# Kernel optimization log

Measured on AMD Instinct MI355X. Metric: run time of the kernel, lower is better.

## Reference

```python
import jax, jax.numpy as jnp
import numpy as np

B, S, D, H = 2, 2048, 2048, 16  # batch, seq, d_model, n_heads
LN_EPS = 1e-6  # flax nn.LayerNorm default


def _layernorm(x, scale):
    mu = jnp.mean(x, axis=-1, keepdims=True)
    var = jnp.var(x, axis=-1, keepdims=True)
    return (x - mu) * jax.lax.rsqrt(var + LN_EPS) * scale


def setup_inputs() -> dict:
    key = jax.random.key(0)
    ks = jax.random.split(key, 5)
    x = jax.random.normal(ks[0], (B, S, D), dtype=jnp.float32)
    # ALiBi-style bias, broadcastable over batch and query positions
    attn_bias = jax.random.normal(ks[1], (1, H, 1, S), dtype=jnp.float32)
    attention_mask = jnp.ones((B, S), dtype=jnp.int32)
    w_qkv = jax.random.normal(ks[2], (D, 3 * D), dtype=jnp.float32) * 0.01
    b_qkv = jnp.zeros((3 * D,), dtype=jnp.float32)
    wo = jax.random.normal(ks[3], (D, D), dtype=jnp.float32) * 0.01
    b_wo = jnp.zeros((D,), dtype=jnp.float32)
    q_ln_scale = jnp.ones((D,), dtype=jnp.float32)
    k_ln_scale = jnp.ones((D,), dtype=jnp.float32)
    return {"x": x, "attn_bias": attn_bias, "attention_mask": attention_mask,
            "w_qkv": w_qkv, "b_qkv": b_qkv, "wo": wo, "b_wo": b_wo,
            "q_ln_scale": q_ln_scale, "k_ln_scale": k_ln_scale}


def reference(x, attn_bias, attention_mask, w_qkv, b_qkv, wo, b_wo, q_ln_scale, k_ln_scale):
    b, s, ds = x.shape
    h = H
    d = ds // h  # head dim
    qkv = jnp.einsum('bsd,df->bsf', x, w_qkv) + b_qkv
    q, k, v = jnp.split(qkv, 3, axis=-1)
    # qk-LayerNorm is over the FULL d_model, before head split (as in source)
    q = _layernorm(q, q_ln_scale)
    k = _layernorm(k, k_ln_scale)
    q = q.reshape(b, s, h, d)
    k = k.reshape(b, s, h, d)
    v = v.reshape(b, s, h, d)
    atw = jnp.einsum('bqhd,bkhd->bhqk', q, k) * jax.lax.rsqrt(jnp.asarray(d, v.dtype))
    atw = atw + attn_bias  # ALiBi bias
    mv = jnp.finfo(atw.dtype).min
    # causal mask [1,1,s,s]
    causal = jnp.tril(jnp.ones((s, s), dtype=bool))[None, None]
    # padding mask: 0 where attended, min where masked
    pad = jnp.where(attention_mask.reshape(b, 1, 1, s) == 1, 0.0, mv).astype(atw.dtype)
    atw = atw + pad
    atw = atw + jnp.where(causal, 0.0, mv).astype(atw.dtype)
    atw = jax.nn.softmax(atw, axis=-1)
    out = jnp.einsum('bhqk,bkhd->bqhd', atw, v).reshape(b, s, ds)
    return jnp.einsum('bsd,de->bse', out, wo) + b_wo
```

## Files before the change

### kernel.cpp

```cpp
#include <hip/hip_runtime.h>
#include <stdint.h>
#include <stddef.h>


typedef __attribute__((ext_vector_type(8))) short bf16x8;
typedef __attribute__((ext_vector_type(4))) float f32x4;

#define MFMA16(a, b, c) __builtin_amdgcn_mfma_f32_16x16x32_bf16((a), (b), (c), 0, 0, 0)

__device__ __forceinline__ void async_copy16(void* lds, const void* g) {
  __builtin_amdgcn_global_load_lds(
      (const __attribute__((address_space(1))) void*)g,
      (__attribute__((address_space(3))) void*)lds, 16, 0, 0);
}

__device__ __forceinline__ short f2bf(float f) {
  union { float f; uint32_t u; } v; v.f = f;
  uint32_t r = (v.u + 0x7fffu + ((v.u >> 16) & 1u)) >> 16;
  return (short)(uint16_t)r;
}

__device__ __forceinline__ float bf2f(short s) {
  union { float f; uint32_t u; } v;
  v.u = ((uint32_t)(uint16_t)s) << 16;
  return v.f;
}

#define ATT_SCALE 0.08838834764831845f
#define VMDRAIN asm volatile("s_waitcnt vmcnt(0)" ::: "memory")

__global__ __launch_bounds__(256) void cvt_f32_bf16(const float* __restrict__ in,
                                                    short* __restrict__ out) {
  size_t i = ((size_t)blockIdx.x * 256 + threadIdx.x) * 8;
  f32x4 a = *(const f32x4*)(in + i);
  f32x4 b = *(const f32x4*)(in + i + 4);
  bf16x8 o;
#pragma unroll
  for (int j = 0; j < 4; ++j) { o[j] = f2bf(a[j]); o[4 + j] = f2bf(b[j]); }
  *(bf16x8*)(out + i) = o;
}

__global__ __launch_bounds__(256) void transpose_cvt(const float* __restrict__ in,
                                                     short* __restrict__ out,
                                                     int R, int C) {
  __shared__ float t[64][65];
  const int tid = threadIdx.x;
  const int c0 = blockIdx.x * 64, r0 = blockIdx.y * 64;
#pragma unroll
  for (int i = 0; i < 16; ++i) {
    int idx = i * 256 + tid;
    int r = idx >> 6, c = idx & 63;
    t[r][c] = in[(size_t)(r0 + r) * C + c0 + c];
  }
  __syncthreads();
#pragma unroll
  for (int i = 0; i < 16; ++i) {
    int idx = i * 256 + tid;
    int cc = idx >> 6, rr = idx & 63;
    out[(size_t)(c0 + cc) * R + r0 + rr] = f2bf(t[rr][cc]);
  }
}

__global__ __launch_bounds__(256) void transpose_v_bf(const short* __restrict__ qkv,
                                                      short* __restrict__ vt) {
  __shared__ short t[64][65];
  const int tid = threadIdx.x;
  const int d0 = blockIdx.x * 64;
  const int s0 = blockIdx.y * 64;
  const int bh = blockIdx.z;
  const int b = bh >> 4, h = bh & 15;
#pragma unroll
  for (int i = 0; i < 16; ++i) {
    int idx = i * 256 + tid;
    int r = idx >> 6, c = idx & 63;
    t[r][c] = qkv[(size_t)(b * 2048 + s0 + r) * 6144 + 4096 + h * 128 + d0 + c];
  }
  __syncthreads();
#pragma unroll
  for (int i = 0; i < 16; ++i) {
    int idx = i * 256 + tid;
    int dd = idx >> 6, ss = idx & 63;
    vt[((size_t)(bh * 128 + d0 + dd)) * 2048 + s0 + ss] = t[ss][dd];
  }
}

__global__ __launch_bounds__(256) void ln_qk(const short* __restrict__ qkv,
                                             const float* __restrict__ qsc,
                                             const float* __restrict__ ksc,
                                             short* __restrict__ q_bf,
                                             short* __restrict__ k_bf) {
  __shared__ float redS[2][4], redQ[2][4];
  const int row = blockIdx.x, tid = threadIdx.x;
  const int lane = tid & 63, wave = tid >> 6;
  const short* base = qkv + (size_t)row * 6144;
#pragma unroll
  for (int part = 0; part < 2; ++part) {
    const short* p = base + part * 2048 + tid * 8;
    bf16x8 v8 = *(const bf16x8*)p;
    float f[8];
#pragma unroll
    for (int j = 0; j < 8; ++j) f[j] = bf2f(v8[j]);
    float s = 0.f, sq = 0.f;
#pragma unroll
    for (int j = 0; j < 8; ++j) { s += f[j]; sq += f[j] * f[j]; }
#pragma unroll
    for (int d = 1; d < 64; d <<= 1) { s += __shfl_xor(s, d); sq += __shfl_xor(sq, d); }
    if (lane == 0) { redS[part][wave] = s; redQ[part][wave] = sq; }
    __syncthreads();
    float tot  = redS[part][0] + redS[part][1] + redS[part][2] + redS[part][3];
    float totq = redQ[part][0] + redQ[part][1] + redQ[part][2] + redQ[part][3];
    float mean = tot * (1.f / 2048.f);
    float var  = totq * (1.f / 2048.f) - mean * mean;
    float rstd = rsqrtf(var + 1e-6f) * (part == 0 ? ATT_SCALE : 1.0f);
    const float* scp = (part == 0 ? qsc : ksc) + tid * 8;
    f32x4 s0 = *(const f32x4*)scp;
    f32x4 s1 = *(const f32x4*)(scp + 4);
    bf16x8 o;
#pragma unroll
    for (int j = 0; j < 4; ++j) {
      o[j]     = f2bf((f[j] - mean) * rstd * s0[j]);
      o[4 + j] = f2bf((f[4 + j] - mean) * rstd * s1[j]);
    }
    short* outp = (part == 0 ? q_bf : k_bf) + (size_t)row * 2048 + tid * 8;
    *(bf16x8*)outp = o;
  }
}

template <typename OutT>
__global__ __launch_bounds__(256, 2) void gemm_bt_bias(const short* __restrict__ A,
                                                       const short* __restrict__ BT,
                                                       const float* __restrict__ bias,
                                                       OutT* __restrict__ C,
                                                       int M, int N, int K) {
  __shared__ alignas(16) short a_lds[128 * 64];
  __shared__ alignas(16) short b_lds[128 * 64];
  const int tid = threadIdx.x;
  const int lane = tid & 63, wave = tid >> 6;
  const int wr = wave >> 1, wc = wave & 1;
  const int tn = blockIdx.x, tm = blockIdx.y;
  const int r15 = lane & 15, hi = lane >> 4;

  const short* Ab = A + (size_t)tm * 128 * K;
  const short* Bb = BT + (size_t)tn * 128 * K;

  f32x4 acc[4][4];
  const f32x4 Z = {0.f, 0.f, 0.f, 0.f};
#pragma unroll
  for (int m = 0; m < 4; ++m)
#pragma unroll
    for (int n = 0; n < 4; ++n) acc[m][n] = Z;

  for (int k0 = 0; k0 < K; k0 += 64) {
    __syncthreads();
#pragma unroll
    for (int j = 0; j < 4; ++j) {
      int c = j * 256 + tid;
      int row = c >> 3;
      int ch = (c & 7) ^ (row & 7);
      async_copy16(&a_lds[c << 3], Ab + (size_t)row * K + k0 + (ch << 3));
      async_copy16(&b_lds[c << 3], Bb + (size_t)row * K + k0 + (ch << 3));
    }
    VMDRAIN;
    __syncthreads();
#pragma unroll
    for (int kk = 0; kk < 2; ++kk) {
      bf16x8 af[4], bfr[4];
#pragma unroll
      for (int m = 0; m < 4; ++m) {
        int row = wr * 64 + m * 16 + r15;
        af[m] = *(const bf16x8*)&a_lds[row * 64 + (((kk * 4 + hi) ^ (row & 7)) << 3)];
      }
#pragma unroll
      for (int n = 0; n < 4; ++n) {
        int row = wc * 64 + n * 16 + r15;
        bfr[n] = *(const bf16x8*)&b_lds[row * 64 + (((kk * 4 + hi) ^ (row & 7)) << 3)];
      }
#pragma unroll
      for (int m = 0; m < 4; ++m)
#pragma unroll
        for (int n = 0; n < 4; ++n)
          acc[m][n] = MFMA16(af[m], bfr[n], acc[m][n]);
    }
  }

  const int r0 = tm * 128 + wr * 64;
  const int c0 = tn * 128 + wc * 64;
#pragma unroll
  for (int n = 0; n < 4; ++n) {
    float bv = bias[c0 + n * 16 + r15];
#pragma unroll
    for (int m = 0; m < 4; ++m) {
#pragma unroll
      for (int r = 0; r < 4; ++r) {
        float val = acc[m][n][r] + bv;
        size_t idx = (size_t)(r0 + m * 16 + hi * 4 + r) * N + c0 + n * 16 + r15;
        if constexpr (sizeof(OutT) == 2) C[idx] = (OutT)f2bf(val);
        else                             C[idx] = val;
      }
    }
  }
}

__global__ __launch_bounds__(256) void attn_fwd(const short* __restrict__ q_bf,
                                                const short* __restrict__ k_bf,
                                                const short* __restrict__ vt,
                                                const float* __restrict__ abias,
                                                const int* __restrict__ amask,
                                                short* __restrict__ out_bf) {
  __shared__ alignas(16) short K_lds[64 * 128];
  __shared__ alignas(16) short V_lds[128 * 64];
  __shared__ alignas(16) short p_lds[4][16 * 64];
  __shared__ float bias_c[2048];

  const int tid = threadIdx.x, lane = tid & 63, wave = tid >> 6;
  const int qt = 31 - blockIdx.x;
  const int h = blockIdx.y, b = blockIdx.z;
  const int r15 = lane & 15, hi = lane >> 4;

  for (int i = tid; i < 2048; i += 256) {
    float bb = abias[h * 2048 + i];
    if (amask[b * 2048 + i] == 0) bb = -1e30f;
    bias_c[i] = bb;
  }

  const int qrow = b * 2048 + qt * 64 + wave * 16 + r15;
  bf16x8 qf[4];
#pragma unroll
  for (int kb = 0; kb < 4; ++kb)
    qf[kb] = *(const bf16x8*)(q_bf + (size_t)qrow * 2048 + h * 128 + kb * 32 + hi * 8);

  f32x4 O[8];
  const f32x4 Z = {0.f, 0.f, 0.f, 0.f};
#pragma unroll
  for (int n = 0; n < 8; ++n) O[n] = Z;
  f32x4 Ol = Z;
  float m_run[4];
#pragma unroll
  for (int r = 0; r < 4; ++r) m_run[r] = -3e38f;

  const short one_bf = (short)0x3F80;
  const bf16x8 ones_f = {one_bf, one_bf, one_bf, one_bf,
                         one_bf, one_bf, one_bf, one_bf};
  const int qg0 = qt * 64 + wave * 16 + hi * 4;
  const int ntiles = qt + 1;

  for (int kt = 0; kt < ntiles; ++kt) {
    __syncthreads();

#pragma unroll
    for (int j = 0; j < 4; ++j) {
      int c = j * 256 + tid;
      int kr = c >> 4, kc = (c & 15) ^ (kr & 7);
      async_copy16(&K_lds[c << 3],
                   k_bf + (size_t)(b * 2048 + kt * 64 + kr) * 2048 + h * 128 + (kc << 3));
      int vr = c >> 3, vc = (c & 7) ^ (vr & 7);
      async_copy16(&V_lds[c << 3],
                   vt + ((size_t)((b * 16 + h) * 128 + vr)) * 2048 + kt * 64 + (vc << 3));
    }
    VMDRAIN;
    __syncthreads();

    f32x4 s[4];
#pragma unroll
    for (int ks = 0; ks < 4; ++ks) {
      s[ks] = Z;
#pragma unroll
      for (int kb = 0; kb < 4; ++kb) {
        int row = ks * 16 + r15;
        int ch = (kb * 4 + hi) ^ (row & 7);
        bf16x8 kf = *(const bf16x8*)&K_lds[row * 128 + ch * 8];
        s[ks] = MFMA16(qf[kb], kf, s[ks]);
      }
    }

    if (kt == qt) {
#pragma unroll
      for (int ks = 0; ks < 4; ++ks) {
        int kg = kt * 64 + ks * 16 + r15;
        float bb = bias_c[kg];
#pragma unroll
        for (int r = 0; r < 4; ++r) {
          float v = s[ks][r] + bb;
          if (kg > qg0 + r) v = -1e30f;
          s[ks][r] = v;
        }
      }
    } else {
#pragma unroll
      for (int ks = 0; ks < 4; ++ks) {
        float bb = bias_c[kt * 64 + ks * 16 + r15];
#pragma unroll
        for (int r = 0; r < 4; ++r) s[ks][r] += bb;
      }
    }

    float corr[4];
#pragma unroll
    for (int r = 0; r < 4; ++r) {
      float mx = fmaxf(fmaxf(s[0][r], s[1][r]), fmaxf(s[2][r], s[3][r]));
      mx = fmaxf(mx, __shfl_xor(mx, 1));
      mx = fmaxf(mx, __shfl_xor(mx, 2));
      mx = fmaxf(mx, __shfl_xor(mx, 4));
      mx = fmaxf(mx, __shfl_xor(mx, 8));
      float mn = fmaxf(m_run[r], mx);
      corr[r] = __expf(m_run[r] - mn);
      m_run[r] = mn;
#pragma unroll
      for (int ks = 0; ks < 4; ++ks) s[ks][r] = __expf(s[ks][r] - mn);
    }
#pragma unroll
    for (int r = 0; r < 4; ++r) {
      Ol[r] *= corr[r];
#pragma unroll
      for (int n = 0; n < 8; ++n) O[n][r] *= corr[r];
    }

    short* pw = &p_lds[wave][0];
#pragma unroll
    for (int r = 0; r < 4; ++r) {
      int q = hi * 4 + r;
      int qs = (q & 7) << 3;
      uint32_t pk0, pk1;
      asm("v_cvt_pk_bf16_f32 %0, %1, %2" : "=v"(pk0) : "v"(s[0][r]), "v"(s[1][r]));
      asm("v_cvt_pk_bf16_f32 %0, %1, %2" : "=v"(pk1) : "v"(s[2][r]), "v"(s[3][r]));
      pw[q * 64 + ((r15) ^ qs)]      = (short)pk0;
      pw[q * 64 + ((16 + r15) ^ qs)] = (short)(pk0 >> 16);
      pw[q * 64 + ((32 + r15) ^ qs)] = (short)pk1;
      pw[q * 64 + ((48 + r15) ^ qs)] = (short)(pk1 >> 16);
    }

    bf16x8 pf[2];
#pragma unroll
    for (int kb = 0; kb < 2; ++kb)
      pf[kb] = *(const bf16x8*)&pw[r15 * 64 + ((kb * 32 + hi * 8) ^ ((r15 & 7) << 3))];

#pragma unroll
    for (int n = 0; n < 8; ++n) {
#pragma unroll
      for (int kb = 0; kb < 2; ++kb) {
        int row = n * 16 + r15;
        int ch = (kb * 4 + hi) ^ (row & 7);
        bf16x8 vf = *(const bf16x8*)&V_lds[row * 64 + ch * 8];
        O[n] = MFMA16(pf[kb], vf, O[n]);
      }
    }
    Ol = MFMA16(pf[0], ones_f, Ol);
    Ol = MFMA16(pf[1], ones_f, Ol);
  }

  float inv[4];
#pragma unroll
  for (int r = 0; r < 4; ++r) inv[r] = 1.0f / Ol[r];
  const int orow = b * 2048 + qt * 64 + wave * 16;
#pragma unroll
  for (int n = 0; n < 8; ++n)
#pragma unroll
    for (int r = 0; r < 4; ++r)
      out_bf[(size_t)(orow + hi * 4 + r) * 2048 + h * 128 + n * 16 + r15] =
          f2bf(O[n][r] * inv[r]);
}

extern "C" void kernel_launch(void* const* d_in, const int* in_sizes, int n_in,
                              void* d_out, int out_size, void* d_ws, size_t ws_size,
                              hipStream_t stream) {
  const float* x     = (const float*)d_in[0];
  const float* abias = (const float*)d_in[1];
  const int*   amask = (const int*)d_in[2];
  const float* w_qkv = (const float*)d_in[3];
  const float* b_qkv = (const float*)d_in[4];
  const float* wo    = (const float*)d_in[5];
  const float* b_wo  = (const float*)d_in[6];
  const float* q_ln  = (const float*)d_in[7];
  const float* k_ln  = (const float*)d_in[8];
  float* out = (float*)d_out;

  char* ws = (char*)d_ws;
  short* x_bf   = (short*)(ws);
  short* wqkvT  = (short*)(ws + 16777216);
  short* woT    = (short*)(ws + 41943040);
  short* q_bf   = (short*)(ws + 50331648);
  short* k_bf   = (short*)(ws + 67108864);
  short* vt     = (short*)(ws + 83886080);
  short* out_bf = (short*)(ws + 100663296);
  short* qkv_bf = (short*)(ws + 117440512);

  cvt_f32_bf16<<<4096, 256, 0, stream>>>(x, x_bf);
  transpose_cvt<<<dim3(96, 32), 256, 0, stream>>>(w_qkv, wqkvT, 2048, 6144);
  transpose_cvt<<<dim3(32, 32), 256, 0, stream>>>(wo, woT, 2048, 2048);
  gemm_bt_bias<short><<<dim3(48, 32), 256, 0, stream>>>(x_bf, wqkvT, b_qkv, qkv_bf,
                                                        4096, 6144, 2048);
  ln_qk<<<4096, 256, 0, stream>>>(qkv_bf, q_ln, k_ln, q_bf, k_bf);
  transpose_v_bf<<<dim3(2, 32, 32), 256, 0, stream>>>(qkv_bf, vt);
  attn_fwd<<<dim3(32, 16, 2), 256, 0, stream>>>(q_bf, k_bf, vt, abias, amask, out_bf);
  gemm_bt_bias<float><<<dim3(16, 32), 256, 0, stream>>>(out_bf, woT, b_wo, out,
                                                        4096, 2048, 2048);
}
```

Baseline: 357.3 us.

## Load K/V fragments directly from global memory instead of staging through LDS

The attention kernel no longer stages K and V tiles into shared memory with async copies and barriers. Each wave now reads its MFMA operands straight from global memory (relying on L2/cache), and reads the bias and mask per tile instead of precomputing a bias array in LDS. This removes the per-tile barriers and LDS traffic, and the lower LDS use may allow more blocks per CU. The cost is that each of the four waves redundantly fetches the same K/V data from global memory, and per-lane loads are strided by row.

```diff
diff --git a/kernel.cpp b/kernel.cpp
--- a/kernel.cpp
+++ b/kernel.cpp
@@ -201,27 +201,18 @@
   }
 }
 
-__global__ __launch_bounds__(256) void attn_fwd(const short* __restrict__ q_bf,
-                                                const short* __restrict__ k_bf,
-                                                const short* __restrict__ vt,
-                                                const float* __restrict__ abias,
-                                                const int* __restrict__ amask,
-                                                short* __restrict__ out_bf) {
-  __shared__ alignas(16) short K_lds[64 * 128];
-  __shared__ alignas(16) short V_lds[128 * 64];
+__global__ __launch_bounds__(256) void attn_fwd2(const short* __restrict__ q_bf,
+                                                 const short* __restrict__ k_bf,
+                                                 const short* __restrict__ vt,
+                                                 const float* __restrict__ abias,
+                                                 const int* __restrict__ amask,
+                                                 short* __restrict__ out_bf) {
   __shared__ alignas(16) short p_lds[4][16 * 64];
-  __shared__ float bias_c[2048];
 
   const int tid = threadIdx.x, lane = tid & 63, wave = tid >> 6;
   const int qt = 31 - blockIdx.x;
   const int h = blockIdx.y, b = blockIdx.z;
   const int r15 = lane & 15, hi = lane >> 4;
-
-  for (int i = tid; i < 2048; i += 256) {
-    float bb = abias[h * 2048 + i];
-    if (amask[b * 2048 + i] == 0) bb = -1e30f;
-    bias_c[i] = bb;
-  }
 
   const int qrow = b * 2048 + qt * 64 + wave * 16 + r15;
   bf16x8 qf[4];
@@ -244,31 +235,21 @@
   const int qg0 = qt * 64 + wave * 16 + hi * 4;
   const int ntiles = qt + 1;
 
+  const short* Kbase = k_bf + ((size_t)(b * 2048)) * 2048 + h * 128;
+  const short* Vbase = vt + ((size_t)((b * 16 + h) * 128)) * 2048;
+  const float* Bbase = abias + (size_t)h * 2048;
+  const int*   Mbase = amask + (size_t)b * 2048;
+
   for (int kt = 0; kt < ntiles; ++kt) {
-    __syncthreads();
-
-#pragma unroll
-    for (int j = 0; j < 4; ++j) {
-      int c = j * 256 + tid;
-      int kr = c >> 4, kc = (c & 15) ^ (kr & 7);
-      async_copy16(&K_lds[c << 3],
-                   k_bf + (size_t)(b * 2048 + kt * 64 + kr) * 2048 + h * 128 + (kc << 3));
-      int vr = c >> 3, vc = (c & 7) ^ (vr & 7);
-      async_copy16(&V_lds[c << 3],
-                   vt + ((size_t)((b * 16 + h) * 128 + vr)) * 2048 + kt * 64 + (vc << 3));
-    }
-    VMDRAIN;
-    __syncthreads();
-
     f32x4 s[4];
 #pragma unroll
     for (int ks = 0; ks < 4; ++ks) {
       s[ks] = Z;
+      const int krow = kt * 64 + ks * 16 + r15;
+      const short* kp = Kbase + (size_t)krow * 2048;
 #pragma unroll
       for (int kb = 0; kb < 4; ++kb) {
-        int row = ks * 16 + r15;
-        int ch = (kb * 4 + hi) ^ (row & 7);
-        bf16x8 kf = *(const bf16x8*)&K_lds[row * 128 + ch * 8];
+        bf16x8 kf = *(const bf16x8*)(kp + (kb * 4 + hi) * 8);
         s[ks] = MFMA16(qf[kb], kf, s[ks]);
       }
     }
@@ -277,7 +258,8 @@
 #pragma unroll
       for (int ks = 0; ks < 4; ++ks) {
         int kg = kt * 64 + ks * 16 + r15;
-        float bb = bias_c[kg];
+        float bb = Bbase[kg];
+        if (Mbase[kg] == 0) bb = -1e30f;
 #pragma unroll
         for (int r = 0; r < 4; ++r) {
           float v = s[ks][r] + bb;
@@ -288,7 +270,9 @@
     } else {
 #pragma unroll
       for (int ks = 0; ks < 4; ++ks) {
-        float bb = bias_c[kt * 64 + ks * 16 + r15];
+        int kg = kt * 64 + ks * 16 + r15;
+        float bb = Bbase[kg];
+        if (Mbase[kg] == 0) bb = -1e30f;
 #pragma unroll
         for (int r = 0; r < 4; ++r) s[ks][r] += bb;
       }
@@ -336,11 +320,11 @@
 
 #pragma unroll
     for (int n = 0; n < 8; ++n) {
+      const int vrow = n * 16 + r15;
+      const short* vp = Vbase + (size_t)vrow * 2048 + kt * 64;
 #pragma unroll
       for (int kb = 0; kb < 2; ++kb) {
-        int row = n * 16 + r15;
-        int ch = (kb * 4 + hi) ^ (row & 7);
-        bf16x8 vf = *(const bf16x8*)&V_lds[row * 64 + ch * 8];
+        bf16x8 vf = *(const bf16x8*)(vp + (kb * 4 + hi) * 8);
         O[n] = MFMA16(pf[kb], vf, O[n]);
       }
     }
@@ -391,7 +375,7 @@
                                                         4096, 6144, 2048);
   ln_qk<<<4096, 256, 0, stream>>>(qkv_bf, q_ln, k_ln, q_bf, k_bf);
   transpose_v_bf<<<dim3(2, 32, 32), 256, 0, stream>>>(qkv_bf, vt);
-  attn_fwd<<<dim3(32, 16, 2), 256, 0, stream>>>(q_bf, k_bf, vt, abias, amask, out_bf);
+  attn_fwd2<<<dim3(32, 16, 2), 256, 0, stream>>>(q_bf, k_bf, vt, abias, amask, out_bf);
   gemm_bt_bias<float><<<dim3(16, 32), 256, 0, stream>>>(out_bf, woT, b_wo, out,
                                                         4096, 2048, 2048);
 }
```

Result: slower. 789.2 us (+120.9%).
